# Optimization experiments

Measured on AMD Instinct MI355X. Metric: run time of the kernel, lower is better.

The kernel has to match this reference:

```python
import jax, jax.numpy as jnp
import numpy as np

N = 50000          # nodes
E = 600000         # edges
D_IN = 256         # input_feat_dim
H1 = 128           # hidden_dim1
H2 = 64            # hidden_dim2
DK = 64            # trs_depth (total key/value depth)
HEADS = 2


def setup_inputs() -> dict:
    key = jax.random.key(0)
    ks = jax.random.split(key, 12)
    inp = {
        "ns_emb": jax.random.normal(ks[0], (N, D_IN), dtype=jnp.float32),
        "edge_rows": jax.random.randint(ks[1], (E,), 0, N, dtype=jnp.int32),
        "edge_cols": jax.random.randint(ks[2], (E,), 0, N, dtype=jnp.int32),
        "edge_vals": jax.random.uniform(ks[3], (E,), dtype=jnp.float32),
        "condition": jax.random.normal(ks[4], (1, 128, H1), dtype=jnp.float32),
        # GCN linear weights (bias=False), stored [in, out]
        "W_hidden": jax.random.normal(ks[5], (D_IN, H1), dtype=jnp.float32) / np.sqrt(D_IN),
        "W_mu": jax.random.normal(ks[6], (H1, H2), dtype=jnp.float32) / np.sqrt(H1),
        "W_var": jax.random.normal(ks[7], (H1, H2), dtype=jnp.float32) / np.sqrt(H1),
        # MultiHeadAttention (bias-free) projections
        "Wq": jax.random.normal(ks[8], (H1, DK), dtype=jnp.float32) / np.sqrt(H1),
        "Wk": jax.random.normal(ks[9], (H1, DK), dtype=jnp.float32) / np.sqrt(H1),
        "Wv": jax.random.normal(ks[10], (H1, DK), dtype=jnp.float32) / np.sqrt(H1),
        "Wo": jax.random.normal(ks[11], (DK, H1), dtype=jnp.float32) / np.sqrt(DK),
    }
    return inp


def _spmm(rows, cols, vals, x):
    # sparse [N,N] @ x  via gather + segment-sum over COO edges
    gathered = vals[:, None] * x[cols]            # [E, d]
    return jax.ops.segment_sum(gathered, rows, num_segments=N)


def _gcn(x, W, rows, cols, vals):
    # dropout is identity in eval mode
    support = jax.nn.leaky_relu(x @ W)            # [N, out]
    out = _spmm(rows, cols, vals, support)        # [N, out]
    return jax.nn.leaky_relu(out)


def _mha(q, kv, Wq, Wk, Wv, Wo):
    # MoEL-style MultiHeadAttention, bias-free, no mask/dropout
    B, Lq, _ = q.shape
    Lk = kv.shape[1]
    dk = DK // HEADS
    Q = (q @ Wq).reshape(B, Lq, HEADS, dk).transpose(0, 2, 1, 3) * (dk ** -0.5)
    K = (kv @ Wk).reshape(B, Lk, HEADS, dk).transpose(0, 2, 1, 3)
    V = (kv @ Wv).reshape(B, Lk, HEADS, dk).transpose(0, 2, 1, 3)
    logits = jnp.einsum("bhqd,bhkd->bhqk", Q, K)
    w = jax.nn.softmax(logits, axis=-1)
    ctx = jnp.einsum("bhqk,bhkd->bhqd", w, V)
    ctx = ctx.transpose(0, 2, 1, 3).reshape(B, Lq, DK)
    return ctx @ Wo, w


def reference(ns_emb, edge_rows, edge_cols, edge_vals, condition,
              W_hidden, W_mu, W_var, Wq, Wk, Wv, Wo):
    hidden = _gcn(ns_emb, W_hidden, edge_rows, edge_cols, edge_vals)   # [N, H1]
    attended, _ = _mha(hidden[None], condition, Wq, Wk, Wv, Wo)        # [1, N, H1]
    h = attended[0]
    mu = _gcn(h, W_mu, edge_rows, edge_cols, edge_vals)                # [N, H2]
    var = _gcn(h, W_var, edge_rows, edge_cols, edge_vals)              # [N, H2]
    return mu, var
```

## Files before the change

kernel.cpp:

```cpp
#include <hip/hip_runtime.h>
#include <hip/hip_bf16.h>
#include <cstdint>


typedef __attribute__((ext_vector_type(8))) short short8;
typedef __attribute__((ext_vector_type(4))) float f32x4;

__device__ __forceinline__ unsigned short f2bf(float f) {
    unsigned int u = __builtin_bit_cast(unsigned int, f);
    u += 0x7fffu + ((u >> 16) & 1u);
    return (unsigned short)(u >> 16);
}
__device__ __forceinline__ float bf2f(unsigned short v) {
    return __builtin_bit_cast(float, (unsigned int)v << 16);
}
__device__ __forceinline__ unsigned int pk2(float a, float b) {
    unsigned int r;
    asm("v_cvt_pk_bf16_f32 %0, %1, %2" : "=v"(r) : "v"(a), "v"(b));
    return r;
}


__global__ __launch_bounds__(256) void hist_prep_kernel(
    const int* __restrict__ rows, int* __restrict__ cnt, int E, int SC,
    const float* __restrict__ Wh, const float* __restrict__ Wq,
    const float* __restrict__ cond,
    const float* __restrict__ Wk, const float* __restrict__ Wv,
    const float* __restrict__ Wo, const float* __restrict__ Wmu,
    const float* __restrict__ Wvar,
    unsigned short* __restrict__ WhT, unsigned short* __restrict__ WqT,
    unsigned short* __restrict__ Ktt, unsigned short* __restrict__ Vt,
    unsigned short* __restrict__ WomT)
{
    const int t = threadIdx.x;
    if ((int)blockIdx.x < SC) {
        const int T = SC * 256;
        const int i0 = blockIdx.x * 256 + t;
        int r[4]; bool ok[4];
#pragma unroll
        for (int k = 0; k < 4; ++k) {
            int idx = i0 + k * T;
            ok[k] = idx < E;
            r[k] = rows[ok[k] ? idx : 0];
        }
#pragma unroll
        for (int k = 0; k < 4; ++k)
            if (ok[k]) atomicAdd(&cnt[r[k]], 1);
        return;
    }
    const int bid = blockIdx.x - SC;
    if (bid < 160) {
        int idx = bid * 256 + t;
        if (idx < 32768) {
            int n = idx & 127, k = idx >> 7;
            WhT[n * 256 + k] = f2bf(Wh[k * 128 + n]);
        } else {
            int i = idx - 32768, n = i & 63, k = i >> 6;
            WqT[n * 128 + k] = f2bf(Wq[k * 64 + n]);
        }
    } else if (bid < 224) {
        int b2 = bid - 160;
        __shared__ float c[2][128];
        c[t >> 7][t & 127] = cond[b2 * 256 + t];
        __syncthreads();
        int j = b2 * 2 + (t >> 7);
        int tl = t & 127;
        const float* W = (tl < 64) ? Wk : Wv;
        int col = tl & 63;
        float acc = 0.f;
#pragma unroll 8
        for (int k = 0; k < 128; ++k) acc = fmaf(c[t >> 7][k], W[k * 64 + col], acc);
        int h = col >> 5, d = col & 31;
        if (tl < 64) Ktt[((size_t)h * 128 + j) * 32 + d] = f2bf(acc * 0.17677669529663687f);
        else         Vt[((size_t)h * 32 + d) * 128 + j] = f2bf(acc);
    } else {
        int wb = bid - 224;
        __shared__ float WoTl[128 * 65];
#pragma unroll
        for (int i = 0; i < 32; ++i) {
            int idx = t + 256 * i;
            int d = idx >> 7, k = idx & 127;
            WoTl[k * 65 + d] = Wo[idx];
        }
        __syncthreads();
        int o = wb * 256 + t;
        int d = o & 63, n = o >> 6;
        const float* W = (n < 64) ? Wmu : Wvar;
        int j = n & 63;
        float acc = 0.f;
#pragma unroll 8
        for (int k = 0; k < 128; ++k) acc = fmaf(WoTl[k * 65 + d], W[k * 64 + j], acc);
        WomT[n * 64 + d] = f2bf(acc);
    }
}


__global__ __launch_bounds__(256) void scan_fused_kernel(
    const int* __restrict__ cnt, int* __restrict__ bsum, int* __restrict__ flag,
    int* __restrict__ row_start, int* __restrict__ cursor, int N, int E)
{
    __shared__ int sh[256];
    const int t = threadIdx.x, b = blockIdx.x;
    const int i = b * 256 + t;
    int v = (i < N) ? cnt[i] : 0;
    sh[t] = v;
    __syncthreads();
    for (int off = 1; off < 256; off <<= 1) {
        int x = (t >= off) ? sh[t - off] : 0;
        __syncthreads();
        sh[t] += x;
        __syncthreads();
    }
    const int incl = sh[t];
    const int aggregate = sh[255];

    if (t == 255) {
        __hip_atomic_store(&bsum[b], aggregate, __ATOMIC_RELAXED, __HIP_MEMORY_SCOPE_AGENT);
        __hip_atomic_store(&flag[b], 1, __ATOMIC_RELEASE, __HIP_MEMORY_SCOPE_AGENT);
    }

    int acc = 0;
    if (t < b) {
        while (__hip_atomic_load(&flag[t], __ATOMIC_ACQUIRE, __HIP_MEMORY_SCOPE_AGENT) == 0) {}
        acc = __hip_atomic_load(&bsum[t], __ATOMIC_RELAXED, __HIP_MEMORY_SCOPE_AGENT);
    }
    __syncthreads();
    sh[t] = acc;
    __syncthreads();
    for (int off = 128; off > 0; off >>= 1) {
        if (t < off) sh[t] += sh[t + off];
        __syncthreads();
    }
    const int boff = sh[0];
    if (i < N) {
        int w = incl - v + boff;
        row_start[i] = w;
        cursor[i] = w;
    }
    if (b == 0 && t == 0) row_start[N] = E;
}


__global__ __launch_bounds__(256) void scatter_gcn1_kernel(
    const int* __restrict__ rows, const int* __restrict__ colsIn,
    const float* __restrict__ valsIn, int* __restrict__ cursor,
    int2* __restrict__ pack, int E, int SC,
    const float* __restrict__ A, const unsigned short* __restrict__ BT,
    unsigned short* __restrict__ C, int M)
{
    __shared__ unsigned short As[128][72];
    __shared__ unsigned short Bs[128][72];

    const int tid = threadIdx.x;

    if ((int)blockIdx.x < SC) {
        const int T = SC * 256;
        const int i0 = blockIdx.x * 256 + tid;
        int r[4], c[4], vb[4]; bool ok[4];
#pragma unroll
        for (int k = 0; k < 4; ++k) {
            int idx = i0 + k * T;
            ok[k] = idx < E;
            int safe = ok[k] ? idx : 0;
            r[k] = rows[safe];
            c[k] = colsIn[safe];
            vb[k] = __float_as_int(valsIn[safe]);
        }
        int pos[4];
#pragma unroll
        for (int k = 0; k < 4; ++k)
            if (ok[k]) pos[k] = atomicAdd(&cursor[r[k]], 1);
#pragma unroll
        for (int k = 0; k < 4; ++k)
            if (ok[k]) pack[pos[k]] = make_int2(c[k], vb[k]);
        return;
    }

    const int lane = tid & 63, wave = tid >> 6;
    const int wm = wave & 1, wn = wave >> 1;
    const int quad = lane >> 4, l16 = lane & 15;
    const int r0 = ((int)blockIdx.x - SC) * 128;

    f32x4 acc[4][4];
#pragma unroll
    for (int mt = 0; mt < 4; ++mt)
#pragma unroll
        for (int nt = 0; nt < 4; ++nt)
#pragma unroll
            for (int r = 0; r < 4; ++r) acc[mt][nt][r] = 0.f;

    for (int kc = 0; kc < 256; kc += 64) {
#pragma unroll
        for (int i = 0; i < 8; ++i) {
            int f = tid + 256 * i;
            int row = f >> 4, kq = (f & 15) << 2;
            int gr = r0 + row;
            if (gr >= M) gr = M - 1;
            float4 v = *reinterpret_cast<const float4*>(&A[(size_t)gr * 256 + kc + kq]);
            unsigned int lo = pk2(v.x, v.y), hi = pk2(v.z, v.w);
            *reinterpret_cast<uint2*>(&As[row][kq]) = make_uint2(lo, hi);
        }
#pragma unroll
        for (int i = 0; i < 4; ++i) {
            int f = tid + 256 * i;
            int n = f >> 3, k8 = (f & 7) << 3;
            *reinterpret_cast<short8*>(&Bs[n][k8]) =
                *reinterpret_cast<const short8*>(&BT[(size_t)n * 256 + kc + k8]);
        }
        __syncthreads();

#pragma unroll
        for (int ks = 0; ks < 2; ++ks) {
            const int koff = ks * 32 + quad * 8;
            short8 a[4], b[4];
#pragma unroll
            for (int mt = 0; mt < 4; ++mt)
                a[mt] = *reinterpret_cast<const short8*>(&As[wm * 64 + mt * 16 + l16][koff]);
#pragma unroll
            for (int nt = 0; nt < 4; ++nt)
                b[nt] = *reinterpret_cast<const short8*>(&Bs[wn * 64 + nt * 16 + l16][koff]);
#pragma unroll
            for (int mt = 0; mt < 4; ++mt)
#pragma unroll
                for (int nt = 0; nt < 4; ++nt)
                    acc[mt][nt] = __builtin_amdgcn_mfma_f32_16x16x32_bf16(
                        a[mt], b[nt], acc[mt][nt], 0, 0, 0);
        }
        __syncthreads();
    }

#pragma unroll
    for (int mt = 0; mt < 4; ++mt)
#pragma unroll
        for (int nt = 0; nt < 4; ++nt) {
            int gc = wn * 64 + nt * 16 + l16;
#pragma unroll
            for (int r = 0; r < 4; ++r) {
                int gr = r0 + wm * 64 + mt * 16 + quad * 4 + r;
                if (gr < M) {
                    float v = acc[mt][nt][r];
                    v = v > 0.f ? v : 0.01f * v;
                    C[(size_t)gr * 128 + gc] = f2bf(v);
                }
            }
        }
}


__global__ __launch_bounds__(256) void attn_muvar_kernel(
    const unsigned short* __restrict__ hidden,
    const unsigned short* __restrict__ WqT,
    const unsigned short* __restrict__ Ktt,
    const unsigned short* __restrict__ Vt,
    const unsigned short* __restrict__ WomT,
    unsigned short* __restrict__ muvar,
    int M)
{
    __shared__ unsigned short Qs[4][16 * 72];
    __shared__ unsigned short Ps[4][16 * 136];
    __shared__ unsigned short Csh[4][16 * 72];

    const int tid = threadIdx.x;
    const int lane = tid & 63, wave = tid >> 6;
    const int quad = lane >> 4, l16 = lane & 15;

    const int strip = blockIdx.x * 4 + wave;
    const int base = strip * 16;
    if (base >= M) return;
    int qrow = base + l16;
    if (qrow >= M) qrow = M - 1;

    unsigned short* Q  = &Qs[wave][0];
    unsigned short* P  = &Ps[wave][0];
    unsigned short* Cl = &Csh[wave][0];

    {
        f32x4 qacc[4];
#pragma unroll
        for (int mt = 0; mt < 4; ++mt)
#pragma unroll
            for (int r = 0; r < 4; ++r) qacc[mt][r] = 0.f;

        short8 hb[4];
#pragma unroll
        for (int ks = 0; ks < 4; ++ks)
            hb[ks] = *reinterpret_cast<const short8*>(
                &hidden[(size_t)qrow * 128 + ks * 32 + quad * 8]);
#pragma unroll
        for (int mt = 0; mt < 4; ++mt)
#pragma unroll
            for (int ks = 0; ks < 4; ++ks) {
                short8 a = *reinterpret_cast<const short8*>(
                    &WqT[(size_t)(mt * 16 + l16) * 128 + ks * 32 + quad * 8]);
                qacc[mt] = __builtin_amdgcn_mfma_f32_16x16x32_bf16(a, hb[ks], qacc[mt], 0, 0, 0);
            }
#pragma unroll
        for (int mt = 0; mt < 4; ++mt) {
            uint2 w;
            w.x = pk2(qacc[mt][0], qacc[mt][1]);
            w.y = pk2(qacc[mt][2], qacc[mt][3]);
            *reinterpret_cast<uint2*>(&Q[l16 * 72 + mt * 16 + quad * 4]) = w;
        }
    }

    f32x4 ctv[2][2];
#pragma unroll
    for (int h = 0; h < 2; ++h)
#pragma unroll
        for (int mt = 0; mt < 2; ++mt)
#pragma unroll
            for (int r = 0; r < 4; ++r) ctv[h][mt][r] = 0.f;

#pragma unroll
    for (int h = 0; h < 2; ++h) {
        f32x4 st[8];
        short8 qb = *reinterpret_cast<const short8*>(&Q[l16 * 72 + h * 32 + quad * 8]);
#pragma unroll
        for (int mt = 0; mt < 8; ++mt) {
            short8 a = *reinterpret_cast<const short8*>(
                &Ktt[(size_t)h * 4096 + (mt * 16 + l16) * 32 + quad * 8]);
            f32x4 z; z[0] = 0.f; z[1] = 0.f; z[2] = 0.f; z[3] = 0.f;
            st[mt] = __builtin_amdgcn_mfma_f32_16x16x32_bf16(a, qb, z, 0, 0, 0);
        }

        float mx = st[0][0];
#pragma unroll
        for (int mt = 0; mt < 8; ++mt)
#pragma unroll
            for (int r = 0; r < 4; ++r) mx = fmaxf(mx, st[mt][r]);
        mx = fmaxf(mx, __shfl_xor(mx, 16, 64));
        mx = fmaxf(mx, __shfl_xor(mx, 32, 64));
        float s = 0.f;
#pragma unroll
        for (int mt = 0; mt < 8; ++mt)
#pragma unroll
            for (int r = 0; r < 4; ++r) {
                float e = __expf(st[mt][r] - mx);
                st[mt][r] = e;
                s += e;
            }
        s += __shfl_xor(s, 16, 64);
        s += __shfl_xor(s, 32, 64);
        float inv = 1.0f / s;

#pragma unroll
        for (int mt = 0; mt < 8; ++mt) {
            uint2 w;
            w.x = pk2(st[mt][0] * inv, st[mt][1] * inv);
            w.y = pk2(st[mt][2] * inv, st[mt][3] * inv);
            *reinterpret_cast<uint2*>(&P[l16 * 136 + mt * 16 + quad * 4]) = w;
        }

#pragma unroll
        for (int ks = 0; ks < 4; ++ks) {
            short8 pb = *reinterpret_cast<const short8*>(&P[l16 * 136 + ks * 32 + quad * 8]);
#pragma unroll
            for (int mt = 0; mt < 2; ++mt) {
                short8 a = *reinterpret_cast<const short8*>(
                    &Vt[(size_t)h * 4096 + (mt * 16 + l16) * 128 + ks * 32 + quad * 8]);
                ctv[h][mt] = __builtin_amdgcn_mfma_f32_16x16x32_bf16(a, pb, ctv[h][mt], 0, 0, 0);
            }
        }
    }

#pragma unroll
    for (int h = 0; h < 2; ++h)
#pragma unroll
        for (int mt = 0; mt < 2; ++mt) {
            uint2 w;
            w.x = pk2(ctv[h][mt][0], ctv[h][mt][1]);
            w.y = pk2(ctv[h][mt][2], ctv[h][mt][3]);
            *reinterpret_cast<uint2*>(&Cl[l16 * 72 + h * 32 + mt * 16 + quad * 4]) = w;
        }

    {
        f32x4 mv[8];
#pragma unroll
        for (int mt = 0; mt < 8; ++mt)
#pragma unroll
            for (int r = 0; r < 4; ++r) mv[mt][r] = 0.f;
        short8 cb[2];
#pragma unroll
        for (int ks = 0; ks < 2; ++ks)
            cb[ks] = *reinterpret_cast<const short8*>(&Cl[l16 * 72 + ks * 32 + quad * 8]);
#pragma unroll
        for (int mt = 0; mt < 8; ++mt)
#pragma unroll
            for (int ks = 0; ks < 2; ++ks) {
                short8 a = *reinterpret_cast<const short8*>(
                    &WomT[(size_t)(mt * 16 + l16) * 64 + ks * 32 + quad * 8]);
                mv[mt] = __builtin_amdgcn_mfma_f32_16x16x32_bf16(a, cb[ks], mv[mt], 0, 0, 0);
            }
        if (base + l16 < M) {
#pragma unroll
            for (int mt = 0; mt < 8; ++mt) {
                float v0 = mv[mt][0], v1 = mv[mt][1], v2 = mv[mt][2], v3 = mv[mt][3];
                v0 = v0 > 0.f ? v0 : 0.01f * v0;
                v1 = v1 > 0.f ? v1 : 0.01f * v1;
                v2 = v2 > 0.f ? v2 : 0.01f * v2;
                v3 = v3 > 0.f ? v3 : 0.01f * v3;
                uint2 w;
                w.x = pk2(v0, v1);
                w.y = pk2(v2, v3);
                *reinterpret_cast<uint2*>(
                    &muvar[(size_t)(base + l16) * 128 + mt * 16 + quad * 4]) = w;
            }
        }
    }
}


template<bool SPLIT, typename OT>
__global__ __launch_bounds__(256) void spmm_kernel(
    const int* __restrict__ row_start, const int2* __restrict__ pack,
    const unsigned short* __restrict__ X,
    OT* __restrict__ out0, OT* __restrict__ out1, int N)
{
    const int wave = threadIdx.x >> 6, lane = threadIdx.x & 63;
    const int r = blockIdx.x * 4 + wave;
    if (r >= N) return;
    int s = __builtin_amdgcn_readfirstlane(row_start[r]);
    int e = __builtin_amdgcn_readfirstlane(row_start[r + 1]);
    const int fo = lane * 2;

    float ax[8], ay[8];
#pragma unroll
    for (int k = 0; k < 8; ++k) { ax[k] = 0.f; ay[k] = 0.f; }

    int i = s;
    for (; i + 8 <= e; i += 8) {
        int2 p[8];
        unsigned int x[8];
#pragma unroll
        for (int k = 0; k < 8; ++k) p[k] = pack[i + k];
#pragma unroll
        for (int k = 0; k < 8; ++k)
            x[k] = *reinterpret_cast<const unsigned int*>(&X[(size_t)p[k].x * 128 + fo]);
#pragma unroll
        for (int k = 0; k < 8; ++k) {
            float v = __int_as_float(p[k].y);
            ax[k] = fmaf(v, bf2f((unsigned short)x[k]), ax[k]);
            ay[k] = fmaf(v, bf2f((unsigned short)(x[k] >> 16)), ay[k]);
        }
    }
    if (i < e) {
        int2 p[8];
        unsigned int x[8];
#pragma unroll
        for (int k = 0; k < 8; ++k) {
            int idx = i + k;
            p[k] = pack[idx < e ? idx : e - 1];
        }
#pragma unroll
        for (int k = 0; k < 8; ++k)
            x[k] = *reinterpret_cast<const unsigned int*>(&X[(size_t)p[k].x * 128 + fo]);
#pragma unroll
        for (int k = 0; k < 8; ++k) {
            float v = (i + k < e) ? __int_as_float(p[k].y) : 0.f;
            ax[k] = fmaf(v, bf2f((unsigned short)x[k]), ax[k]);
            ay[k] = fmaf(v, bf2f((unsigned short)(x[k] >> 16)), ay[k]);
        }
    }

    float ox = ((ax[0] + ax[1]) + (ax[2] + ax[3])) + ((ax[4] + ax[5]) + (ax[6] + ax[7]));
    float oy = ((ay[0] + ay[1]) + (ay[2] + ay[3])) + ((ay[4] + ay[5]) + (ay[6] + ay[7]));
    ox = ox > 0.f ? ox : 0.01f * ox;
    oy = oy > 0.f ? oy : 0.01f * oy;

    if constexpr (!SPLIT) {
        unsigned int w = (unsigned int)f2bf(ox) | ((unsigned int)f2bf(oy) << 16);
        *reinterpret_cast<unsigned int*>(&out0[(size_t)r * 128 + fo]) = w;
    } else {
        if (lane < 32) {
            *reinterpret_cast<float2*>(&out0[(size_t)r * 64 + fo]) = make_float2(ox, oy);
        } else {
            *reinterpret_cast<float2*>(&out1[(size_t)r * 64 + (fo - 64)]) = make_float2(ox, oy);
        }
    }
}


extern "C" void kernel_launch(void* const* d_in, const int* in_sizes, int n_in,
                              void* d_out, int out_size, void* d_ws, size_t ws_size,
                              hipStream_t stream)
{
    const float* ns_emb   = (const float*)d_in[0];
    const int*   erows    = (const int*)d_in[1];
    const int*   ecols    = (const int*)d_in[2];
    const float* evals    = (const float*)d_in[3];
    const float* cond     = (const float*)d_in[4];
    const float* W_hidden = (const float*)d_in[5];
    const float* W_mu     = (const float*)d_in[6];
    const float* W_var    = (const float*)d_in[7];
    const float* Wq       = (const float*)d_in[8];
    const float* Wk       = (const float*)d_in[9];
    const float* Wv       = (const float*)d_in[10];
    const float* Wo       = (const float*)d_in[11];

    const int N = in_sizes[0] / 256;
    const int E = in_sizes[1];

    typedef unsigned short bf16;
    uint8_t* p = (uint8_t*)d_ws;
    auto alloc = [&](size_t bytes) {
        uint8_t* r = p;
        p += (bytes + 255) & ~(size_t)255;
        return r;
    };
    bf16* support1 = (bf16*)alloc(sizeof(bf16) * (size_t)N * 128);
    bf16* hidden   = (bf16*)alloc(sizeof(bf16) * (size_t)N * 128);
    bf16* muvarb   = (bf16*)alloc(sizeof(bf16) * (size_t)N * 128);
    bf16* Ktt      = (bf16*)alloc(sizeof(bf16) * 2 * 128 * 32);
    bf16* Vt       = (bf16*)alloc(sizeof(bf16) * 2 * 32 * 128);
    bf16* WhT      = (bf16*)alloc(sizeof(bf16) * 128 * 256);
    bf16* WqT      = (bf16*)alloc(sizeof(bf16) * 64 * 128);
    bf16* WomT     = (bf16*)alloc(sizeof(bf16) * 128 * 64);
    int*  cnt      = (int*)alloc(sizeof(int) * N);
    int*  flag     = (int*)alloc(sizeof(int) * 256);
    int*  bsum     = (int*)alloc(sizeof(int) * 256);
    int*  row_start= (int*)alloc(sizeof(int) * (N + 1));
    int*  cursor   = (int*)alloc(sizeof(int) * N);
    int2* pack     = (int2*)alloc(sizeof(int2) * E);

    const int SC = (E + 1023) / 1024;
    const int nb = (N + 255) / 256;
    const int mb128 = (N + 127) / 128;

    size_t zbytes = (size_t)((uint8_t*)flag - (uint8_t*)cnt) + sizeof(int) * 256;
    hipMemsetAsync(cnt, 0, zbytes, stream);

    hist_prep_kernel<<<SC + 256, 256, 0, stream>>>(erows, cnt, E, SC,
                                                   W_hidden, Wq, cond, Wk, Wv,
                                                   Wo, W_mu, W_var,
                                                   WhT, WqT, Ktt, Vt, WomT);

    scan_fused_kernel<<<nb, 256, 0, stream>>>(cnt, bsum, flag, row_start, cursor, N, E);

    scatter_gcn1_kernel<<<SC + mb128, 256, 0, stream>>>(
        erows, ecols, evals, cursor, pack, E, SC,
        ns_emb, WhT, support1, N);

    const int sblocks = (N + 3) / 4;
    spmm_kernel<false, bf16><<<sblocks, 256, 0, stream>>>(
        row_start, pack, support1, hidden, nullptr, N);

    const int strips = (N + 15) / 16;
    const int ablocks = (strips + 3) / 4;
    attn_muvar_kernel<<<ablocks, 256, 0, stream>>>(hidden, WqT, Ktt, Vt,
                                                   WomT, muvarb, N);

    spmm_kernel<true, float><<<sblocks, 256, 0, stream>>>(
        row_start, pack, muvarb, (float*)d_out, (float*)d_out + (size_t)N * 64, N);
}
```

Baseline: 276.9 us.

## Split scatter from GCN1 GEMM and partition scatter by row range

The fused scatter+GEMM kernel is split into two launches. The scatter now runs 8 passes, each keeping only edges whose row falls in one eighth of the node range, so the cursor atomics and pack writes of each group land in a narrower memory region with better locality. The histogram goes back to one edge per thread. In exchange, the rows array is read 8 times, the scatter no longer overlaps with the GEMM, and one extra kernel launch is added.

```diff
diff --git a/kernel.cpp b/kernel.cpp
--- a/kernel.cpp
+++ b/kernel.cpp
@@ -22,7 +22,7 @@
 
 
 __global__ __launch_bounds__(256) void hist_prep_kernel(
-    const int* __restrict__ rows, int* __restrict__ cnt, int E, int SC,
+    const int* __restrict__ rows, int* __restrict__ cnt, int E, int HB,
     const float* __restrict__ Wh, const float* __restrict__ Wq,
     const float* __restrict__ cond,
     const float* __restrict__ Wk, const float* __restrict__ Wv,
@@ -33,22 +33,12 @@
     unsigned short* __restrict__ WomT)
 {
     const int t = threadIdx.x;
-    if ((int)blockIdx.x < SC) {
-        const int T = SC * 256;
-        const int i0 = blockIdx.x * 256 + t;
-        int r[4]; bool ok[4];
-#pragma unroll
-        for (int k = 0; k < 4; ++k) {
-            int idx = i0 + k * T;
-            ok[k] = idx < E;
-            r[k] = rows[ok[k] ? idx : 0];
-        }
-#pragma unroll
-        for (int k = 0; k < 4; ++k)
-            if (ok[k]) atomicAdd(&cnt[r[k]], 1);
+    if ((int)blockIdx.x < HB) {
+        int i = blockIdx.x * 256 + t;
+        if (i < E) atomicAdd(&cnt[rows[i]], 1);
         return;
     }
-    const int bid = blockIdx.x - SC;
+    const int bid = blockIdx.x - HB;
     if (bid < 160) {
         int idx = bid * 256 + t;
         if (idx < 32768) {
@@ -141,10 +131,47 @@
 }
 
 
-__global__ __launch_bounds__(256) void scatter_gcn1_kernel(
+__global__ __launch_bounds__(256) void scatter_kernel(
     const int* __restrict__ rows, const int* __restrict__ colsIn,
     const float* __restrict__ valsIn, int* __restrict__ cursor,
-    int2* __restrict__ pack, int E, int SC,
+    int2* __restrict__ pack, int E, int GB, int bsize, int N)
+{
+    const int g = blockIdx.x & 7;
+    const int j = blockIdx.x >> 3;
+    const int lo = g * bsize;
+    const int hi = min(lo + bsize, N);
+    const int T = GB * 256;
+    const int i0 = j * 256 + threadIdx.x;
+
+    int r[4]; bool ok[4];
+#pragma unroll
+    for (int k = 0; k < 4; ++k) {
+        int idx = i0 + k * T;
+        bool in = idx < E;
+        int rr = rows[in ? idx : 0];
+        ok[k] = in && rr >= lo && rr < hi;
+        r[k] = rr;
+    }
+    int c[4], vb[4];
+#pragma unroll
+    for (int k = 0; k < 4; ++k) {
+        int idx = i0 + k * T;
+        if (ok[k]) {
+            c[k] = colsIn[idx];
+            vb[k] = __float_as_int(valsIn[idx]);
+        }
+    }
+    int pos[4];
+#pragma unroll
+    for (int k = 0; k < 4; ++k)
+        if (ok[k]) pos[k] = atomicAdd(&cursor[r[k]], 1);
+#pragma unroll
+    for (int k = 0; k < 4; ++k)
+        if (ok[k]) pack[pos[k]] = make_int2(c[k], vb[k]);
+}
+
+
+__global__ __launch_bounds__(256) void gcn1_gemm(
     const float* __restrict__ A, const unsigned short* __restrict__ BT,
     unsigned short* __restrict__ C, int M)
 {
@@ -152,34 +179,10 @@
     __shared__ unsigned short Bs[128][72];
 
     const int tid = threadIdx.x;
-
-    if ((int)blockIdx.x < SC) {
-        const int T = SC * 256;
-        const int i0 = blockIdx.x * 256 + tid;
-        int r[4], c[4], vb[4]; bool ok[4];
-#pragma unroll
-        for (int k = 0; k < 4; ++k) {
-            int idx = i0 + k * T;
-            ok[k] = idx < E;
-            int safe = ok[k] ? idx : 0;
-            r[k] = rows[safe];
-            c[k] = colsIn[safe];
-            vb[k] = __float_as_int(valsIn[safe]);
-        }
-        int pos[4];
-#pragma unroll
-        for (int k = 0; k < 4; ++k)
-            if (ok[k]) pos[k] = atomicAdd(&cursor[r[k]], 1);
-#pragma unroll
-        for (int k = 0; k < 4; ++k)
-            if (ok[k]) pack[pos[k]] = make_int2(c[k], vb[k]);
-        return;
-    }
-
     const int lane = tid & 63, wave = tid >> 6;
     const int wm = wave & 1, wn = wave >> 1;
     const int quad = lane >> 4, l16 = lane & 15;
-    const int r0 = ((int)blockIdx.x - SC) * 128;
+    const int r0 = blockIdx.x * 128;
 
     f32x4 acc[4][4];
 #pragma unroll
@@ -522,23 +525,26 @@
     int*  cursor   = (int*)alloc(sizeof(int) * N);
     int2* pack     = (int2*)alloc(sizeof(int2) * E);
 
-    const int SC = (E + 1023) / 1024;
+    const int HB = (E + 255) / 256;
     const int nb = (N + 255) / 256;
     const int mb128 = (N + 127) / 128;
+    const int GB = (E + 1023) / 1024;
+    const int bsize = (N + 7) / 8;
 
     size_t zbytes = (size_t)((uint8_t*)flag - (uint8_t*)cnt) + sizeof(int) * 256;
     hipMemsetAsync(cnt, 0, zbytes, stream);
 
-    hist_prep_kernel<<<SC + 256, 256, 0, stream>>>(erows, cnt, E, SC,
+    hist_prep_kernel<<<HB + 256, 256, 0, stream>>>(erows, cnt, E, HB,
                                                    W_hidden, Wq, cond, Wk, Wv,
                                                    Wo, W_mu, W_var,
                                                    WhT, WqT, Ktt, Vt, WomT);
 
     scan_fused_kernel<<<nb, 256, 0, stream>>>(cnt, bsum, flag, row_start, cursor, N, E);
 
-    scatter_gcn1_kernel<<<SC + mb128, 256, 0, stream>>>(
-        erows, ecols, evals, cursor, pack, E, SC,
-        ns_emb, WhT, support1, N);
+    scatter_kernel<<<8 * GB, 256, 0, stream>>>(erows, ecols, evals, cursor,
+                                               pack, E, GB, bsize, N);
+
+    gcn1_gemm<<<mb128, 256, 0, stream>>>(ns_emb, WhT, support1, N);
 
     const int sblocks = (N + 3) / 4;
     spmm_kernel<false, bf16><<<sblocks, 256, 0, stream>>>(
```

Result: no change. 278.4 us (+0.6%).
